# Optimization experiments

Measured on AMD Instinct MI355X. Metric: run time of the kernel, lower is better.

The kernel has to match this reference:

```python
import jax, jax.numpy as jnp
import numpy as np


def _dct1d(x, norm='ortho'):
    """DCT-II over the last axis via FFT (Makhoul's permutation trick)."""
    N = x.shape[-1]
    # even indices forward, odd indices reversed
    v = jnp.concatenate([x[..., ::2], x[..., 1::2][..., ::-1]], axis=-1)
    Vc = jnp.fft.fft(v, axis=-1)  # complex
    k = -jnp.arange(N, dtype=x.dtype) * (np.pi / (2.0 * N))
    W_r = jnp.cos(k)
    W_i = jnp.sin(k)
    V = Vc.real * W_r - Vc.imag * W_i
    if norm == 'ortho':
        scale = jnp.full((N,), 1.0 / (np.sqrt(N / 2.0) * 2.0), dtype=x.dtype)
        scale = scale.at[0].set(1.0 / (np.sqrt(N) * 2.0))
        V = V * scale
    return 2.0 * V


def _dct2d(x, norm='ortho'):
    X1 = _dct1d(x, norm=norm)                       # DCT over W
    X2 = _dct1d(jnp.swapaxes(X1, -1, -2), norm=norm)  # DCT over H
    return jnp.swapaxes(X2, -1, -2)


def setup_inputs() -> dict:
    key = jax.random.key(0)
    x = jax.random.normal(key, (8, 32, 512, 512), dtype=jnp.float32)
    return {"x": x}


def reference(x):
    return _dct2d(x, norm='ortho')
```

## Files before the change

kernel.cpp:

```cpp
#include <hip/hip_runtime.h>
#include <hip/hip_bf16.h>

typedef __attribute__((ext_vector_type(8))) short short8;
typedef __attribute__((ext_vector_type(4))) float f32x4;
typedef __attribute__((ext_vector_type(4))) float float4v;
typedef __attribute__((ext_vector_type(8))) unsigned short ushort8;

__device__ __forceinline__ unsigned short f2bf(float f) {
    union { float f; unsigned u; } x; x.f = f;
    unsigned r = x.u + 0x7FFFu + ((x.u >> 16) & 1u);
    return (unsigned short)(r >> 16);
}

__global__ __launch_bounds__(256) void make_dct_mat(unsigned short* __restrict__ Cm) {
    int idx = blockIdx.x * 256 + threadIdx.x;
    int k = idx >> 9;
    int n = idx & 511;
    int m = (k * (2 * n + 1)) & 2047;
    float ang = (3.14159265358979323846f / 1024.0f) * (float)m;
    float s = (k == 0) ? 0.04419417382415922f : 0.0625f;
    Cm[idx] = f2bf(s * cosf(ang));
}

#define GLD16(g, l) __builtin_amdgcn_global_load_lds( \
    (const __attribute__((address_space(1))) void*)(g), \
    (__attribute__((address_space(3))) void*)(l), 16, 0, 0)
#define BAR()    asm volatile("s_barrier" ::: "memory")
#define VMCNT(n) asm volatile("s_waitcnt vmcnt(" #n ")" ::: "memory")
#define LGKM0()  asm volatile("s_waitcnt lgkmcnt(0)" ::: "memory")

template <bool B_IS_F32, bool OUT_F32>
__device__ __forceinline__ void dct_gemm_body(
    const unsigned short* __restrict__ A,
    const void* __restrict__ Ball,
    void* __restrict__ Dall)
{
    __shared__ unsigned short As[2][2][2][4096];
    __shared__ unsigned short Bs[2][2][2][4096];

    int wg  = blockIdx.x;
    int cpx = gridDim.x >> 3;
    int swz = (wg & 7) * cpx + (wg >> 3);
    int img = swz >> 2;
    int R0  = ((swz >> 1) & 1) * 256;
    int C0  = (swz & 1) * 256;

    int t    = threadIdx.x;
    int lane = t & 63;
    int wid  = t >> 6;
    int wm   = wid >> 2;
    int wn   = wid & 3;
    int l15  = lane & 15;
    const int roff = ((lane >> 4) ^ ((lane >> 1) & 3)) * 8;

    const size_t imgoff = (size_t)img * (512 * 512);

    const int sXor = ((t & 3) ^ ((t >> 3) & 3)) * 8;
    const unsigned short* gA = A
        + (size_t)(R0 + (t >> 8) * 128 + ((t >> 2) & 63)) * 512 + sXor;
    const int bRow = C0 + ((t >> 7) & 3) * 64 + ((t >> 2) & 31);
    const unsigned short* gB16 = nullptr;
    const float* gBf = nullptr;
    if constexpr (B_IS_F32)
        gBf = (const float*)Ball + imgoff + (size_t)bRow * 512 + sXor;
    else
        gB16 = (const unsigned short*)Ball + imgoff + (size_t)bRow * 512 + sXor;

    auto stageA = [&](int d, int kt, int h) {
        GLD16(gA + (size_t)h * 64 * 512 + kt * 64,      &As[d][h][0][t * 8]);
        GLD16(gA + (size_t)h * 64 * 512 + kt * 64 + 32, &As[d][h][1][t * 8]);
    };
    auto stageB = [&](int d, int kt, int h) {
        GLD16(gB16 + (size_t)h * 32 * 512 + kt * 64,      &Bs[d][h][0][t * 8]);
        GLD16(gB16 + (size_t)h * 32 * 512 + kt * 64 + 32, &Bs[d][h][1][t * 8]);
    };
    float4v rbA[4], rbB[4];
    auto loadB = [&](float4v* rb, int kt, int h) {
        const float* p = gBf + (size_t)h * 32 * 512 + kt * 64;
        rb[0] = *(const float4v*)(p);      rb[1] = *(const float4v*)(p + 4);
        rb[2] = *(const float4v*)(p + 32); rb[3] = *(const float4v*)(p + 36);
    };
    auto writeB = [&](int d, int h, const float4v* rb) {
        #pragma unroll
        for (int ks = 0; ks < 2; ++ks) {
            union { ushort8 u8; __hip_bfloat162 h2[4]; } u;
            u.h2[0] = __float22bfloat162_rn(float2{rb[2*ks].x,   rb[2*ks].y});
            u.h2[1] = __float22bfloat162_rn(float2{rb[2*ks].z,   rb[2*ks].w});
            u.h2[2] = __float22bfloat162_rn(float2{rb[2*ks+1].x, rb[2*ks+1].y});
            u.h2[3] = __float22bfloat162_rn(float2{rb[2*ks+1].z, rb[2*ks+1].w});
            *(ushort8*)(&Bs[d][h][ks][t * 8]) = u.u8;
        }
    };

    short8 avA[4][2], avB[4][2], bvA[2][2], bvB[2][2];
    auto readA = [&](short8 av[4][2], int d, int mh) {
        #pragma unroll
        for (int mq = 0; mq < 4; ++mq)
            #pragma unroll
            for (int ks = 0; ks < 2; ++ks)
                av[mq][ks] = *(const short8*)(
                    &As[d][mh][ks][(wm * 64 + mq * 16 + l15) * 32 + roff]);
    };
    auto readB = [&](short8 bv[2][2], int d, int nh) {
        #pragma unroll
        for (int nq = 0; nq < 2; ++nq)
            #pragma unroll
            for (int ks = 0; ks < 2; ++ks)
                bv[nq][ks] = *(const short8*)(
                    &Bs[d][nh][ks][(wn * 32 + nq * 16 + l15) * 32 + roff]);
    };

    f32x4 acc[8][4] = {};
    auto mfmaQ = [&](short8 av[4][2], short8 bv[2][2], int mh, int nh) {
        __builtin_amdgcn_s_setprio(1);
        #pragma unroll
        for (int mq = 0; mq < 4; ++mq)
            #pragma unroll
            for (int nq = 0; nq < 2; ++nq)
                #pragma unroll
                for (int ks = 0; ks < 2; ++ks)
                    acc[mh*4+mq][nh*2+nq] = __builtin_amdgcn_mfma_f32_16x16x32_bf16(
                        av[mq][ks], bv[nq][ks], acc[mh*4+mq][nh*2+nq], 0, 0, 0);
        __builtin_amdgcn_s_setprio(0);
    };

    if constexpr (B_IS_F32) {
        stageA(0, 0, 0);
        loadB(rbA, 0, 0);
        loadB(rbB, 0, 1);
        stageA(0, 0, 1);
        VMCNT(6);
        writeB(0, 0, rbA);
        VMCNT(2);
        writeB(0, 1, rbB);
        LGKM0();
        BAR();
    } else {
        stageA(0, 0, 0); stageB(0, 0, 0); stageB(0, 0, 1); stageA(0, 0, 1);
        VMCNT(4);
        BAR();
    }

    #pragma unroll
    for (int kt = 0; kt < 8; ++kt) {
        const int d = kt & 1, e = d ^ 1;
        readA(avA, d, 0); readB(bvA, d, 0);
        if constexpr (B_IS_F32) {
            if (kt < 7) loadB(rbA, kt + 1, 0);
        } else {
            if (kt < 7) { stageA(e, kt + 1, 0); VMCNT(4); }
            else        { VMCNT(2); }
        }
        BAR(); LGKM0();
        mfmaQ(avA, bvA, 0, 0);
        BAR();
        readB(bvB, d, 1);
        if constexpr (B_IS_F32) {
            if (kt < 7) { loadB(rbB, kt + 1, 1); VMCNT(8); }
            else        { VMCNT(0); }
        } else {
            if (kt < 7) { stageB(e, kt + 1, 0); VMCNT(4); }
            else        { VMCNT(0); }
        }
        BAR(); LGKM0();
        mfmaQ(avA, bvB, 0, 1);
        BAR();
        readA(avB, d, 1);
        if constexpr (B_IS_F32) {
            if (kt < 7) { VMCNT(4);
                          writeB(e, 0, rbA);
                          stageA(e, kt + 1, 0); }
        } else {
            if (kt < 7) { stageB(e, kt + 1, 1); VMCNT(4); }
        }
        BAR(); LGKM0();
        mfmaQ(avB, bvB, 1, 1);
        BAR();
        if constexpr (B_IS_F32) {
            if (kt < 7) { VMCNT(2);
                          writeB(e, 1, rbB);
                          stageA(e, kt + 1, 1);
                          VMCNT(2); }
        } else {
            if (kt < 7) { stageA(e, kt + 1, 1); VMCNT(4); }
        }
        BAR(); LGKM0();
        mfmaQ(avB, bvA, 1, 0);
        BAR();
    }

    int r0 = R0 + wm * 128 + (lane >> 4) * 4;
    int c0 = C0 + wn * 64 + l15;
    if constexpr (OUT_F32) {
        float* D = (float*)Dall + imgoff;
        #pragma unroll
        for (int m = 0; m < 8; ++m)
            #pragma unroll
            for (int n = 0; n < 4; ++n)
                #pragma unroll
                for (int r = 0; r < 4; ++r)
                    D[(size_t)(r0 + (m >> 2) * 64 + (m & 3) * 16 + r) * 512
                      + c0 + (n >> 1) * 32 + (n & 1) * 16] = acc[m][n][r];
    } else {
        unsigned short* D = (unsigned short*)Dall + imgoff;
        #pragma unroll
        for (int m = 0; m < 8; ++m)
            #pragma unroll
            for (int n = 0; n < 4; ++n)
                #pragma unroll
                for (int r = 0; r < 4; ++r)
                    D[(size_t)(r0 + (m >> 2) * 64 + (m & 3) * 16 + r) * 512
                      + c0 + (n >> 1) * 32 + (n & 1) * 16] = f2bf(acc[m][n][r]);
    }
}

__global__ __launch_bounds__(512, 2) void dct_gemm_s1(
    const unsigned short* __restrict__ A, const float* __restrict__ B,
    unsigned short* __restrict__ D) {
    dct_gemm_body<true, false>(A, B, D);
}

__global__ __launch_bounds__(512, 2) void dct_gemm_s2(
    const unsigned short* __restrict__ A, const unsigned short* __restrict__ B,
    float* __restrict__ D) {
    dct_gemm_body<false, true>(A, B, D);
}

extern "C" void kernel_launch(void* const* d_in, const int* in_sizes, int n_in,
                              void* d_out, int out_size, void* d_ws, size_t ws_size,
                              hipStream_t stream) {
    const float* x = (const float*)d_in[0];
    float* out = (float*)d_out;

    unsigned short* Cm = (unsigned short*)d_ws;
    unsigned short* Tm = (unsigned short*)((char*)d_ws + (1 << 20));

    int nimg = in_sizes[0] / (512 * 512);

    make_dct_mat<<<dim3(1024), dim3(256), 0, stream>>>(Cm);
    dct_gemm_s1<<<dim3(nimg * 4), dim3(512), 0, stream>>>(Cm, x, Tm);
    dct_gemm_s2<<<dim3(nimg * 4), dim3(512), 0, stream>>>(Cm, Tm, out);
}
```

Baseline: 256.0 us.

## Stream fp32 B tiles in half-size chunks to cut register staging

Stage one of the fp32 input operand in four 32-column chunks, using two 2-vector register buffers instead of two 4-vector buffers. Each chunk is loaded, converted to bf16 and written to LDS in a rolling schedule spread across the four MFMA phases. Compiler memory barriers pin the order of the async LDS loads so the vmcnt waits stay correct. The aim is to lower VGPR pressure and spread conversion work more evenly, at the cost of a more delicate wait-count schedule that risks hazards, such as the last chunk being written into the current buffer at the start of the next iteration.

```diff
diff --git a/kernel.cpp b/kernel.cpp
--- a/kernel.cpp
+++ b/kernel.cpp
@@ -28,6 +28,7 @@
 #define BAR()    asm volatile("s_barrier" ::: "memory")
 #define VMCNT(n) asm volatile("s_waitcnt vmcnt(" #n ")" ::: "memory")
 #define LGKM0()  asm volatile("s_waitcnt lgkmcnt(0)" ::: "memory")
+#define MEMORD() asm volatile("" ::: "memory")
 
 template <bool B_IS_F32, bool OUT_F32>
 __device__ __forceinline__ void dct_gemm_body(
@@ -74,22 +75,20 @@
         GLD16(gB16 + (size_t)h * 32 * 512 + kt * 64,      &Bs[d][h][0][t * 8]);
         GLD16(gB16 + (size_t)h * 32 * 512 + kt * 64 + 32, &Bs[d][h][1][t * 8]);
     };
-    float4v rbA[4], rbB[4];
-    auto loadB = [&](float4v* rb, int kt, int h) {
-        const float* p = gBf + (size_t)h * 32 * 512 + kt * 64;
-        rb[0] = *(const float4v*)(p);      rb[1] = *(const float4v*)(p + 4);
-        rb[2] = *(const float4v*)(p + 32); rb[3] = *(const float4v*)(p + 36);
-    };
-    auto writeB = [&](int d, int h, const float4v* rb) {
-        #pragma unroll
-        for (int ks = 0; ks < 2; ++ks) {
-            union { ushort8 u8; __hip_bfloat162 h2[4]; } u;
-            u.h2[0] = __float22bfloat162_rn(float2{rb[2*ks].x,   rb[2*ks].y});
-            u.h2[1] = __float22bfloat162_rn(float2{rb[2*ks].z,   rb[2*ks].w});
-            u.h2[2] = __float22bfloat162_rn(float2{rb[2*ks+1].x, rb[2*ks+1].y});
-            u.h2[3] = __float22bfloat162_rn(float2{rb[2*ks+1].z, rb[2*ks+1].w});
-            *(ushort8*)(&Bs[d][h][ks][t * 8]) = u.u8;
-        }
+
+    float4v cU[2], cV[2];
+    auto loadChunk = [&](float4v* cb, int kt, int h, int ks) {
+        const float* p = gBf + (size_t)h * 32 * 512 + kt * 64 + ks * 32;
+        cb[0] = *(const float4v*)(p);
+        cb[1] = *(const float4v*)(p + 4);
+    };
+    auto writeChunk = [&](int dbuf, int h, int ks, const float4v* cb) {
+        union { ushort8 u8; __hip_bfloat162 h2[4]; } u;
+        u.h2[0] = __float22bfloat162_rn(float2{cb[0].x, cb[0].y});
+        u.h2[1] = __float22bfloat162_rn(float2{cb[0].z, cb[0].w});
+        u.h2[2] = __float22bfloat162_rn(float2{cb[1].x, cb[1].y});
+        u.h2[3] = __float22bfloat162_rn(float2{cb[1].z, cb[1].w});
+        *(ushort8*)(&Bs[dbuf][h][ks][t * 8]) = u.u8;
     };
 
     short8 avA[4][2], avB[4][2], bvA[2][2], bvB[2][2];
@@ -125,18 +124,23 @@
     };
 
     if constexpr (B_IS_F32) {
-        stageA(0, 0, 0);
-        loadB(rbA, 0, 0);
-        loadB(rbB, 0, 1);
+        loadChunk(cU, 0, 0, 0);   MEMORD();
+        stageA(0, 0, 0);          MEMORD();
+        loadChunk(cV, 0, 0, 1);
+        VMCNT(4);
+        writeChunk(0, 0, 0, cU);
+        loadChunk(cU, 0, 1, 0);   MEMORD();
         stageA(0, 0, 1);
-        VMCNT(6);
-        writeB(0, 0, rbA);
-        VMCNT(2);
-        writeB(0, 1, rbB);
+        VMCNT(4);
+        writeChunk(0, 0, 1, cV);
+        loadChunk(cV, 0, 1, 1);
+        VMCNT(4);
+        writeChunk(0, 1, 0, cU);
         LGKM0();
         BAR();
     } else {
-        stageA(0, 0, 0); stageB(0, 0, 0); stageB(0, 0, 1); stageA(0, 0, 1);
+        stageA(0, 0, 0); MEMORD(); stageB(0, 0, 0); MEMORD();
+        stageB(0, 0, 1); MEMORD(); stageA(0, 0, 1);
         VMCNT(4);
         BAR();
     }
@@ -146,7 +150,11 @@
         const int d = kt & 1, e = d ^ 1;
         readA(avA, d, 0); readB(bvA, d, 0);
         if constexpr (B_IS_F32) {
-            if (kt < 7) loadB(rbA, kt + 1, 0);
+            if (kt < 7) { loadChunk(cU, kt + 1, 0, 0); MEMORD();
+                          stageA(e, kt + 1, 0);
+                          VMCNT(4); }
+            else        { VMCNT(0); }
+            writeChunk(d, 1, 1, cV);
         } else {
             if (kt < 7) { stageA(e, kt + 1, 0); VMCNT(4); }
             else        { VMCNT(2); }
@@ -156,8 +164,9 @@
         BAR();
         readB(bvB, d, 1);
         if constexpr (B_IS_F32) {
-            if (kt < 7) { loadB(rbB, kt + 1, 1); VMCNT(8); }
-            else        { VMCNT(0); }
+            if (kt < 7) { loadChunk(cV, kt + 1, 0, 1);
+                          VMCNT(4);
+                          writeChunk(e, 0, 0, cU); }
         } else {
             if (kt < 7) { stageB(e, kt + 1, 0); VMCNT(4); }
             else        { VMCNT(0); }
@@ -167,9 +176,10 @@
         BAR();
         readA(avB, d, 1);
         if constexpr (B_IS_F32) {
-            if (kt < 7) { VMCNT(4);
-                          writeB(e, 0, rbA);
-                          stageA(e, kt + 1, 0); }
+            if (kt < 7) { loadChunk(cU, kt + 1, 1, 0); MEMORD();
+                          stageA(e, kt + 1, 1);
+                          VMCNT(4);
+                          writeChunk(e, 0, 1, cV); }
         } else {
             if (kt < 7) { stageB(e, kt + 1, 1); VMCNT(4); }
         }
@@ -177,10 +187,9 @@
         mfmaQ(avB, bvB, 1, 1);
         BAR();
         if constexpr (B_IS_F32) {
-            if (kt < 7) { VMCNT(2);
-                          writeB(e, 1, rbB);
-                          stageA(e, kt + 1, 1);
-                          VMCNT(2); }
+            if (kt < 7) { loadChunk(cV, kt + 1, 1, 1);
+                          VMCNT(4);
+                          writeChunk(e, 1, 0, cU); }
         } else {
             if (kt < 7) { stageA(e, kt + 1, 1); VMCNT(4); }
         }
```

After: 250.5 us (median of 2 runs). 1.02x faster.

## Rewrite stage-1 DCT GEMM with fp32 LDS staging and triple-buffered pipeline

Applied to the files above, without the earlier changes.

Stage 1 now has its own kernel. It stages fp32 x tiles directly into LDS via global_load_lds, instead of loading them into registers, converting, and writing them to LDS. The new kernel converts to bf16 at LDS-read time, uses a 512x128 output tile with k-step 32, and triple-buffers with a single barrier per k-step. The aim is to remove register round-trips and extra barriers from the fp32 input path. It costs more LDS space and repeats the fp32-to-bf16 conversion for each warp that reads the same data. Stage 2 is de-templated, with compiler memory-ordering barriers added between the prologue loads.

```diff
diff --git a/kernel.cpp b/kernel.cpp
--- a/kernel.cpp
+++ b/kernel.cpp
@@ -28,12 +28,104 @@
 #define BAR()    asm volatile("s_barrier" ::: "memory")
 #define VMCNT(n) asm volatile("s_waitcnt vmcnt(" #n ")" ::: "memory")
 #define LGKM0()  asm volatile("s_waitcnt lgkmcnt(0)" ::: "memory")
-
-template <bool B_IS_F32, bool OUT_F32>
-__device__ __forceinline__ void dct_gemm_body(
-    const unsigned short* __restrict__ A,
-    const void* __restrict__ Ball,
-    void* __restrict__ Dall)
+#define MEMORD() asm volatile("" ::: "memory")
+
+__global__ __launch_bounds__(512, 2) void dct_gemm_s1(
+    const unsigned short* __restrict__ A, const float* __restrict__ B,
+    unsigned short* __restrict__ D)
+{
+    __shared__ unsigned short As[3][4][128 * 32];
+    __shared__ float          Bf[3][128 * 32];
+
+    int wg  = blockIdx.x;
+    int cpx = gridDim.x >> 3;
+    int swz = (wg & 7) * cpx + (wg >> 3);
+    int img = swz >> 2;
+    int C0  = (swz & 3) * 128;
+
+    int t    = threadIdx.x;
+    int lane = t & 63;
+    int wid  = t >> 6;
+    int wm   = wid >> 1;
+    int wn   = wid & 1;
+    int l15  = lane & 15;
+    int q    = lane >> 4;
+
+    const size_t imgoff = (size_t)img * (512 * 512);
+
+    const int aslotG = ((t & 3) ^ ((t >> 3) & 3)) * 8;
+    const unsigned short* gA = A + (size_t)(t >> 2) * 512 + aslotG;
+    const int bslotG = ((t & 7) ^ ((t >> 3) & 7)) * 4;
+    const float* gB = B + imgoff + (size_t)(C0 + (t >> 3)) * 512 + bslotG;
+
+    auto stage = [&](int sl, int kt) {
+        #pragma unroll
+        for (int ms = 0; ms < 4; ++ms)
+            GLD16(gA + (size_t)ms * 128 * 512 + kt * 32, &As[sl][ms][t * 8]);
+        GLD16(gB + kt * 32,                     &Bf[sl][t * 4]);
+        GLD16(gB + kt * 32 + (size_t)64 * 512,  &Bf[sl][2048 + t * 4]);
+    };
+
+    const int aroff = ((lane >> 4) ^ ((lane >> 1) & 3)) * 8;
+    const int bs0 = ((2 * q)     ^ (lane & 7)) * 4;
+    const int bs1 = ((2 * q + 1) ^ (lane & 7)) * 4;
+
+    f32x4 acc[8][4] = {};
+
+    stage(0, 0);
+    stage(1, 1);
+    VMCNT(6);
+    BAR();
+
+    #pragma unroll 4
+    for (int kt = 0; kt < 16; ++kt) {
+        const int sl = kt % 3;
+        if (kt < 14) stage((kt + 2) % 3, kt + 2);
+
+        short8 av[8], bv[4];
+        #pragma unroll
+        for (int m = 0; m < 8; ++m)
+            av[m] = *(const short8*)(&As[sl][wm][(m * 16 + l15) * 32 + aroff]);
+        #pragma unroll
+        for (int n = 0; n < 4; ++n) {
+            int brow = wn * 64 + n * 16 + l15;
+            float4v fa = *(const float4v*)(&Bf[sl][brow * 32 + bs0]);
+            float4v fb = *(const float4v*)(&Bf[sl][brow * 32 + bs1]);
+            union { short8 s8; __hip_bfloat162 h2[4]; } u;
+            u.h2[0] = __float22bfloat162_rn(float2{fa.x, fa.y});
+            u.h2[1] = __float22bfloat162_rn(float2{fa.z, fa.w});
+            u.h2[2] = __float22bfloat162_rn(float2{fb.x, fb.y});
+            u.h2[3] = __float22bfloat162_rn(float2{fb.z, fb.w});
+            bv[n] = u.s8;
+        }
+        __builtin_amdgcn_s_setprio(1);
+        #pragma unroll
+        for (int m = 0; m < 8; ++m)
+            #pragma unroll
+            for (int n = 0; n < 4; ++n)
+                acc[m][n] = __builtin_amdgcn_mfma_f32_16x16x32_bf16(
+                                av[m], bv[n], acc[m][n], 0, 0, 0);
+        __builtin_amdgcn_s_setprio(0);
+
+        if (kt < 14)      { VMCNT(6); BAR(); }
+        else if (kt == 14){ VMCNT(0); BAR(); }
+    }
+
+    unsigned short* Dp = D + imgoff;
+    int r0 = wm * 128 + q * 4;
+    int c0 = C0 + wn * 64 + l15;
+    #pragma unroll
+    for (int m = 0; m < 8; ++m)
+        #pragma unroll
+        for (int n = 0; n < 4; ++n)
+            #pragma unroll
+            for (int r = 0; r < 4; ++r)
+                Dp[(size_t)(r0 + m * 16 + r) * 512 + c0 + n * 16] = f2bf(acc[m][n][r]);
+}
+
+__global__ __launch_bounds__(512, 2) void dct_gemm_s2(
+    const unsigned short* __restrict__ A, const unsigned short* __restrict__ B,
+    float* __restrict__ D)
 {
     __shared__ unsigned short As[2][2][2][4096];
     __shared__ unsigned short Bs[2][2][2][4096];
@@ -59,12 +151,8 @@
     const unsigned short* gA = A
         + (size_t)(R0 + (t >> 8) * 128 + ((t >> 2) & 63)) * 512 + sXor;
     const int bRow = C0 + ((t >> 7) & 3) * 64 + ((t >> 2) & 31);
-    const unsigned short* gB16 = nullptr;
-    const float* gBf = nullptr;
-    if constexpr (B_IS_F32)
-        gBf = (const float*)Ball + imgoff + (size_t)bRow * 512 + sXor;
-    else
-        gB16 = (const unsigned short*)Ball + imgoff + (size_t)bRow * 512 + sXor;
+    const unsigned short* gB16 =
+        B + imgoff + (size_t)bRow * 512 + sXor;
 
     auto stageA = [&](int d, int kt, int h) {
         GLD16(gA + (size_t)h * 64 * 512 + kt * 64,      &As[d][h][0][t * 8]);
@@ -73,23 +161,6 @@
     auto stageB = [&](int d, int kt, int h) {
         GLD16(gB16 + (size_t)h * 32 * 512 + kt * 64,      &Bs[d][h][0][t * 8]);
         GLD16(gB16 + (size_t)h * 32 * 512 + kt * 64 + 32, &Bs[d][h][1][t * 8]);
-    };
-    float4v rbA[4], rbB[4];
-    auto loadB = [&](float4v* rb, int kt, int h) {
-        const float* p = gBf + (size_t)h * 32 * 512 + kt * 64;
-        rb[0] = *(const float4v*)(p);      rb[1] = *(const float4v*)(p + 4);
-        rb[2] = *(const float4v*)(p + 32); rb[3] = *(const float4v*)(p + 36);
-    };
-    auto writeB = [&](int d, int h, const float4v* rb) {
-        #pragma unroll
-        for (int ks = 0; ks < 2; ++ks) {
-            union { ushort8 u8; __hip_bfloat162 h2[4]; } u;
-            u.h2[0] = __float22bfloat162_rn(float2{rb[2*ks].x,   rb[2*ks].y});
-            u.h2[1] = __float22bfloat162_rn(float2{rb[2*ks].z,   rb[2*ks].w});
-            u.h2[2] = __float22bfloat162_rn(float2{rb[2*ks+1].x, rb[2*ks+1].y});
-            u.h2[3] = __float22bfloat162_rn(float2{rb[2*ks+1].z, rb[2*ks+1].w});
-            *(ushort8*)(&Bs[d][h][ks][t * 8]) = u.u8;
-        }
     };
 
     short8 avA[4][2], avB[4][2], bvA[2][2], bvB[2][2];
@@ -124,106 +195,48 @@
         __builtin_amdgcn_s_setprio(0);
     };
 
-    if constexpr (B_IS_F32) {
-        stageA(0, 0, 0);
-        loadB(rbA, 0, 0);
-        loadB(rbB, 0, 1);
-        stageA(0, 0, 1);
-        VMCNT(6);
-        writeB(0, 0, rbA);
-        VMCNT(2);
-        writeB(0, 1, rbB);
-        LGKM0();
-        BAR();
-    } else {
-        stageA(0, 0, 0); stageB(0, 0, 0); stageB(0, 0, 1); stageA(0, 0, 1);
-        VMCNT(4);
-        BAR();
-    }
+    stageA(0, 0, 0); MEMORD(); stageB(0, 0, 0); MEMORD();
+    stageB(0, 0, 1); MEMORD(); stageA(0, 0, 1);
+    VMCNT(4);
+    BAR();
 
     #pragma unroll
     for (int kt = 0; kt < 8; ++kt) {
         const int d = kt & 1, e = d ^ 1;
         readA(avA, d, 0); readB(bvA, d, 0);
-        if constexpr (B_IS_F32) {
-            if (kt < 7) loadB(rbA, kt + 1, 0);
-        } else {
-            if (kt < 7) { stageA(e, kt + 1, 0); VMCNT(4); }
-            else        { VMCNT(2); }
-        }
+        if (kt < 7) { stageA(e, kt + 1, 0); VMCNT(4); }
+        else        { VMCNT(2); }
         BAR(); LGKM0();
         mfmaQ(avA, bvA, 0, 0);
         BAR();
         readB(bvB, d, 1);
-        if constexpr (B_IS_F32) {
-            if (kt < 7) { loadB(rbB, kt + 1, 1); VMCNT(8); }
-            else        { VMCNT(0); }
-        } else {
-            if (kt < 7) { stageB(e, kt + 1, 0); VMCNT(4); }
-            else        { VMCNT(0); }
-        }
+        if (kt < 7) { stageB(e, kt + 1, 0); VMCNT(4); }
+        else        { VMCNT(0); }
         BAR(); LGKM0();
         mfmaQ(avA, bvB, 0, 1);
         BAR();
         readA(avB, d, 1);
-        if constexpr (B_IS_F32) {
-            if (kt < 7) { VMCNT(4);
-                          writeB(e, 0, rbA);
-                          stageA(e, kt + 1, 0); }
-        } else {
-            if (kt < 7) { stageB(e, kt + 1, 1); VMCNT(4); }
-        }
+        if (kt < 7) { stageB(e, kt + 1, 1); VMCNT(4); }
         BAR(); LGKM0();
         mfmaQ(avB, bvB, 1, 1);
         BAR();
-        if constexpr (B_IS_F32) {
-            if (kt < 7) { VMCNT(2);
-                          writeB(e, 1, rbB);
-                          stageA(e, kt + 1, 1);
-                          VMCNT(2); }
-        } else {
-            if (kt < 7) { stageA(e, kt + 1, 1); VMCNT(4); }
-        }
+        if (kt < 7) { stageA(e, kt + 1, 1); VMCNT(4); }
         BAR(); LGKM0();
         mfmaQ(avB, bvA, 1, 0);
         BAR();
     }
 
+    float* Dp = D + imgoff;
     int r0 = R0 + wm * 128 + (lane >> 4) * 4;
     int c0 = C0 + wn * 64 + l15;
-    if constexpr (OUT_F32) {
-        float* D = (float*)Dall + imgoff;
-        #pragma unroll
-        for (int m = 0; m < 8; ++m)
-            #pragma unroll
-            for (int n = 0; n < 4; ++n)
-                #pragma unroll
-                for (int r = 0; r < 4; ++r)
-                    D[(size_t)(r0 + (m >> 2) * 64 + (m & 3) * 16 + r) * 512
-                      + c0 + (n >> 1) * 32 + (n & 1) * 16] = acc[m][n][r];
-    } else {
-        unsigned short* D = (unsigned short*)Dall + imgoff;
-        #pragma unroll
-        for (int m = 0; m < 8; ++m)
-            #pragma unroll
-            for (int n = 0; n < 4; ++n)
-                #pragma unroll
-                for (int r = 0; r < 4; ++r)
-                    D[(size_t)(r0 + (m >> 2) * 64 + (m & 3) * 16 + r) * 512
-                      + c0 + (n >> 1) * 32 + (n & 1) * 16] = f2bf(acc[m][n][r]);
-    }
-}
-
-__global__ __launch_bounds__(512, 2) void dct_gemm_s1(
-    const unsigned short* __restrict__ A, const float* __restrict__ B,
-    unsigned short* __restrict__ D) {
-    dct_gemm_body<true, false>(A, B, D);
-}
-
-__global__ __launch_bounds__(512, 2) void dct_gemm_s2(
-    const unsigned short* __restrict__ A, const unsigned short* __restrict__ B,
-    float* __restrict__ D) {
-    dct_gemm_body<false, true>(A, B, D);
+    #pragma unroll
+    for (int m = 0; m < 8; ++m)
+        #pragma unroll
+        for (int n = 0; n < 4; ++n)
+            #pragma unroll
+            for (int r = 0; r < 4; ++r)
+                Dp[(size_t)(r0 + (m >> 2) * 64 + (m & 3) * 16 + r) * 512
+                   + c0 + (n >> 1) * 32 + (n & 1) * 16] = acc[m][n][r];
 }
 
 extern "C" void kernel_launch(void* const* d_in, const int* in_sizes, int n_in,
```

Result: no change. 259.8 us (+1.5%).
